# Performance work log

Hardware: AMD Instinct MI355X
Metric: run time of the kernel (lower is better)

Reference implementation:

```python
import jax, jax.numpy as jnp
import numpy as np

C = 1.0          # curvature (c_in == c_out)
MIN = 1e-15      # min_norm clamp (HGCN Hyperboloid)
PROJ_EPS = 4e-3  # proj eps for float32 (HGCN)
MAX_NORM = 1e3   # max tangent norm clamp in expmap
N, D = 262144, 256


def _proj(x, c):
    # project back onto hyperboloid: recompute time coordinate
    K = 1.0 / c
    y = x[..., 1:]
    x0 = jnp.sqrt(jnp.clip(K + jnp.sum(y * y, -1, keepdims=True), PROJ_EPS))
    return jnp.concatenate([x0, y], -1)


def _expmap0(u, c):
    sqrtK = (1.0 / c) ** 0.5
    d = u[..., 1:]
    n = jnp.clip(jnp.linalg.norm(d, axis=-1, keepdims=True), MIN)
    theta = n / sqrtK
    x = jnp.concatenate([sqrtK * jnp.cosh(theta), sqrtK * jnp.sinh(theta) * d / n], -1)
    return _proj(x, c)


def _logmap0(x, c):
    sqrtK = (1.0 / c) ** 0.5
    y = x[..., 1:]
    yn = jnp.clip(jnp.linalg.norm(y, axis=-1, keepdims=True), MIN)
    theta = jnp.arccosh(jnp.clip(x[..., :1] / sqrtK, 1.0 + 1e-7))
    return jnp.concatenate([jnp.zeros_like(theta), sqrtK * theta * y / yn], -1)


def _proj_tan(u, x, c):
    ux = jnp.sum(x[..., 1:] * u[..., 1:], -1, keepdims=True)
    u0 = ux / jnp.clip(x[..., :1], MIN)
    return jnp.concatenate([u0, u[..., 1:]], -1)


def _expmap(u, x, c):
    sqrtK = (1.0 / c) ** 0.5
    mdot = -u[..., :1] ** 2 + jnp.sum(u[..., 1:] ** 2, -1, keepdims=True)  # Minkowski <u,u>
    normu = jnp.minimum(jnp.sqrt(jnp.clip(mdot, 0.0)), MAX_NORM)
    theta = jnp.clip(normu / sqrtK, MIN)
    return _proj(jnp.cosh(theta) * x + jnp.sinh(theta) * u / theta, c)


def _transp0(x, u, c):
    # parallel transport of tangent u from the origin to x
    sqrtK = (1.0 / c) ** 0.5
    x0 = x[..., :1]
    y = x[..., 1:]
    yn = jnp.clip(jnp.linalg.norm(y, axis=-1, keepdims=True), MIN)
    yhat = y / yn
    v = jnp.concatenate([-yn, (sqrtK - x0) * yhat], -1)
    alpha = jnp.sum(yhat * u[..., 1:], -1, keepdims=True) / sqrtK
    return _proj_tan(u - alpha * v, x, c)


def _zero0(u):
    # proj_tan0: zero out the time coordinate
    return jnp.concatenate([jnp.zeros_like(u[..., :1]), u[..., 1:]], -1)


def _layernorm(t, g, b, eps=1e-5):
    mu = jnp.mean(t, -1, keepdims=True)
    var = jnp.var(t, -1, keepdims=True)
    return (t - mu) * jax.lax.rsqrt(var + eps) * g + b


def setup_inputs() -> dict:
    key = jax.random.key(0)
    k1, k2, k3, k4, k5 = jax.random.split(key, 5)
    # point on the hyperboloid: expmap0 of a tangent vector at origin
    u = 0.1 * jax.random.normal(k1, (N, D), dtype=jnp.float32)
    h = _expmap0(_zero0(u), C)
    # xavier_uniform with gain 0.25 for the linear weight
    bound = 0.25 * float(np.sqrt(6.0 / (D + D)))
    W = jax.random.uniform(k2, (D, D), dtype=jnp.float32, minval=-bound, maxval=bound)
    bias = 0.01 * jax.random.normal(k3, (1, D), dtype=jnp.float32)
    gamma = 1.0 + 0.1 * jax.random.normal(k4, (D - 1,), dtype=jnp.float32)
    beta = 0.01 * jax.random.normal(k5, (D - 1,), dtype=jnp.float32)
    return {"h": h, "W": W, "bias": bias, "gamma": gamma, "beta": beta}


def reference(h, W, bias, gamma, beta):
    # HypNorm: logmap0 -> LayerNorm over spatial dims -> expmap0
    t = _logmap0(h, C)
    t = jnp.concatenate([t[..., :1], _layernorm(t[..., 1:], gamma, beta)], -1)
    h1 = _expmap0(t, C)
    # HypLinear: logmap0 -> GEMM -> proj_tan0 -> expmap0 -> bias transport + expmap
    x = _logmap0(h1, C)
    x = x @ W.T
    x = _expmap0(_zero0(x), C)
    b = jnp.broadcast_to(bias, x.shape)
    b = _transp0(x, _zero0(b), C)
    res = _expmap(b, x, C)
    # HypAct: logmap0 -> relu -> proj_tan0 -> expmap0
    xt = jax.nn.relu(_logmap0(res, C))
    return _expmap0(_zero0(xt), C)
```

## Files before the change

kernel.cpp:

```cpp
#include <hip/hip_runtime.h>
#include <hip/hip_bf16.h>
#include <math.h>


#define MINV 1e-15f

typedef __bf16 bf16x8 __attribute__((ext_vector_type(8)));
typedef __bf16 bf16x4 __attribute__((ext_vector_type(4)));
typedef float floatx4 __attribute__((ext_vector_type(4)));

__global__ __launch_bounds__(256) void prep_kernel(const float* __restrict__ W,
                                                   const float* __restrict__ bias,
                                                   __bf16* __restrict__ Wb,
                                                   float* __restrict__ scal) {
  int b = blockIdx.x;
  if (b < 64) {
    int idx = b * 1024 + threadIdx.x * 4;
    int j = idx >> 8;
    float4 w;
    if (j < 255) w = *(const float4*)(W + idx + 256);
    else w = make_float4(0.f, 0.f, 0.f, 0.f);
    bf16x4 o;
    o[0] = (__bf16)w.x; o[1] = (__bf16)w.y; o[2] = (__bf16)w.z; o[3] = (__bf16)w.w;
    *(bf16x4*)(Wb + idx) = o;
  } else if (threadIdx.x < 64) {
    int l = threadIdx.x;
    float4 bv = *(const float4*)(bias + l * 4);
    float s = bv.x * bv.x + bv.y * bv.y + bv.z * bv.z + bv.w * bv.w;
    if (l == 0) s -= bv.x * bv.x;
    for (int m = 1; m < 64; m <<= 1) s += __shfl_xor(s, m);
    if (l == 0) {
      float nb = sqrtf(s);
      float normu = fminf(nb, 1000.0f);
      float th = fmaxf(normu, MINV);
      scal[0] = coshf(th);
      scal[1] = sinhf(th) / th;
      scal[2] = s;
    }
  }
}

__global__ __launch_bounds__(256, 4) void hnn_kernel(const float* __restrict__ h,
                                                     const __bf16* __restrict__ Wb,
                                                     const float* __restrict__ bias,
                                                     const float* __restrict__ gamma,
                                                     const float* __restrict__ beta,
                                                     const float* __restrict__ scal,
                                                     float* __restrict__ out) {
  __shared__ __bf16 Xs[64][264];
  __shared__ __align__(16) float gs[256];
  __shared__ __align__(16) float bs[256];
  __shared__ float partA[64][4];
  __shared__ float partB[64][4];
  __shared__ float rowAB[64][2];
  __shared__ float partX[64][4];
  __shared__ float rowS[64];

  const int tid = threadIdx.x;
  const int wave = tid >> 6;
  const int lane = tid & 63;
  const int lane16 = lane & 15;
  const int quad = lane >> 4;
  const int rowBlock = blockIdx.x * 64;

  float4 hv[4][4];
#pragma unroll
  for (int it = 0; it < 4; ++it) {
    const int row = rowBlock + wave * 16 + it * 4 + quad;
    const float4* hp = (const float4*)(h + row * 256 + lane16 * 16);
    hv[it][0] = hp[0]; hv[it][1] = hp[1]; hv[it][2] = hp[2]; hv[it][3] = hp[3];
  }

  if (tid < 255) { gs[tid + 1] = gamma[tid]; bs[tid + 1] = beta[tid]; }
  else { gs[0] = 0.f; bs[0] = 0.f; }
  __syncthreads();

  float4 gv[4], bv[4];
#pragma unroll
  for (int q = 0; q < 4; ++q) {
    gv[q] = *(const float4*)(gs + lane16 * 16 + q * 4);
    bv[q] = *(const float4*)(bs + lane16 * 16 + q * 4);
  }

#pragma unroll
  for (int it = 0; it < 4; ++it) {
    const int lrow = wave * 16 + it * 4 + quad;
    float vals[16] = {hv[it][0].x, hv[it][0].y, hv[it][0].z, hv[it][0].w,
                      hv[it][1].x, hv[it][1].y, hv[it][1].z, hv[it][1].w,
                      hv[it][2].x, hv[it][2].y, hv[it][2].z, hv[it][2].w,
                      hv[it][3].x, hv[it][3].y, hv[it][3].z, hv[it][3].w};
    float s1l = 0.f, s2l = 0.f;
#pragma unroll
    for (int i = 0; i < 16; ++i) { s1l += vals[i]; s2l += vals[i] * vals[i]; }
    if (lane16 == 0) { s1l -= vals[0]; s2l -= vals[0] * vals[0]; }
#pragma unroll
    for (int m = 1; m < 16; m <<= 1) {
      s1l += __shfl_xor(s1l, m);
      s2l += __shfl_xor(s2l, m);
    }
    float h0 = __shfl(vals[0], lane & 48);
    float yn = fmaxf(sqrtf(s2l), MINV);
    float xc = fmaxf(h0, 1.0f + 1e-7f);
    float theta = __logf(xc + sqrtf(xc * xc - 1.0f));
    float s = theta / yn;
    float mu = s * s1l * (1.0f / 255.0f);
    float var = s * s * (s2l * (1.0f / 255.0f)) - mu * mu;
    float rstd = rsqrtf(var + 1e-5f);
    float a = s * rstd;
    float bshift = -mu * rstd;
    bf16x8 o0, o1;
#pragma unroll
    for (int q = 0; q < 4; ++q) {
      float4 g4 = gv[q];
      float4 b4 = bv[q];
      float t0 = (a * vals[q * 4 + 0] + bshift) * g4.x + b4.x;
      float t1 = (a * vals[q * 4 + 1] + bshift) * g4.y + b4.y;
      float t2 = (a * vals[q * 4 + 2] + bshift) * g4.z + b4.z;
      float t3 = (a * vals[q * 4 + 3] + bshift) * g4.w + b4.w;
      if (q < 2) {
        o0[q * 4 + 0] = (__bf16)t0; o0[q * 4 + 1] = (__bf16)t1;
        o0[q * 4 + 2] = (__bf16)t2; o0[q * 4 + 3] = (__bf16)t3;
      } else {
        o1[(q - 2) * 4 + 0] = (__bf16)t0; o1[(q - 2) * 4 + 1] = (__bf16)t1;
        o1[(q - 2) * 4 + 2] = (__bf16)t2; o1[(q - 2) * 4 + 3] = (__bf16)t3;
      }
    }
    *(bf16x8*)(&Xs[lrow][lane16 * 16]) = o0;
    *(bf16x8*)(&Xs[lrow][lane16 * 16 + 8]) = o1;
  }
  __syncthreads();

  floatx4 acc[4][4];
#pragma unroll
  for (int rt = 0; rt < 4; ++rt)
#pragma unroll
    for (int jt = 0; jt < 4; ++jt) acc[rt][jt] = (floatx4){0.f, 0.f, 0.f, 0.f};

  const int colBase = wave * 64;
  const __bf16* wbase = Wb + (colBase + lane16) * 256 + quad * 8;
  const __bf16* xbase = &Xs[lane16][quad * 8];

#pragma unroll
  for (int kk = 0; kk < 8; ++kk) {
    bf16x8 bfr[4], afr[4];
#pragma unroll
    for (int jt = 0; jt < 4; ++jt)
      bfr[jt] = *(const bf16x8*)(wbase + jt * 4096 + kk * 32);
#pragma unroll
    for (int rt = 0; rt < 4; ++rt)
      afr[rt] = *(const bf16x8*)(xbase + rt * 4224 + kk * 32);
#pragma unroll
    for (int rt = 0; rt < 4; ++rt)
#pragma unroll
      for (int jt = 0; jt < 4; ++jt)
        acc[rt][jt] = __builtin_amdgcn_mfma_f32_16x16x32_bf16(afr[rt], bfr[jt],
                                                              acc[rt][jt], 0, 0, 0);
  }

  float bb1[4];
#pragma unroll
  for (int jt = 0; jt < 4; ++jt) {
    int c = colBase + jt * 16 + lane16;
    bb1[jt] = (c < 255) ? bias[c + 1] : 0.f;
  }

#pragma unroll
  for (int rt = 0; rt < 4; ++rt) {
#pragma unroll
    for (int e = 0; e < 4; ++e) {
      float sv2 = 0.f, svb = 0.f;
#pragma unroll
      for (int jt = 0; jt < 4; ++jt) {
        float v = acc[rt][jt][e];
        sv2 += v * v;
        svb += v * bb1[jt];
      }
#pragma unroll
      for (int m = 1; m < 16; m <<= 1) {
        sv2 += __shfl_xor(sv2, m);
        svb += __shfl_xor(svb, m);
      }
      if (lane16 == 0) {
        int r = rt * 16 + quad * 4 + e;
        partA[r][wave] = sv2;
        partB[r][wave] = svb;
      }
    }
  }
  __syncthreads();

  if (tid < 64) {
    float sv2 = partA[tid][0] + partA[tid][1] + partA[tid][2] + partA[tid][3];
    float svb = partB[tid][0] + partB[tid][1] + partB[tid][2] + partB[tid][3];
    const float c1 = scal[0];
    const float s1s = scal[1];
    const float tb2 = scal[2];
    float n = fmaxf(sqrtf(sv2), MINV);
    float inv_n = 1.0f / n;
    float alpha = svb * inv_n;
    float ex = __expf(n);
    float iex = 1.0f / ex;
    float ch = 0.5f * (ex + iex), sh = 0.5f * (ex - iex);
    float beta_ = c1 * sh + s1s * alpha * (ch - 1.0f);
    float rn2 = beta_ * beta_ + 2.0f * beta_ * s1s * alpha + s1s * s1s * tb2;
    float rn = sqrtf(fmaxf(rn2, 0.f));
    float res0 = sqrtf(1.0f + rn2);
    float th3 = __logf(res0 + rn);
    float sc3 = th3 / fmaxf(rn, MINV);
    rowAB[tid][0] = sc3 * beta_ * inv_n;
    rowAB[tid][1] = sc3 * s1s;
  }
  __syncthreads();

#pragma unroll
  for (int rt = 0; rt < 4; ++rt) {
#pragma unroll
    for (int e = 0; e < 4; ++e) {
      int r = rt * 16 + quad * 4 + e;
      float Ar = rowAB[r][0];
      float Br = rowAB[r][1];
      float sx2 = 0.f;
#pragma unroll
      for (int jt = 0; jt < 4; ++jt) {
        float x = fmaxf(Ar * acc[rt][jt][e] + Br * bb1[jt], 0.f);
        acc[rt][jt][e] = x;
        sx2 += x * x;
      }
#pragma unroll
      for (int m = 1; m < 16; m <<= 1) sx2 += __shfl_xor(sx2, m);
      if (lane16 == 0) partX[r][wave] = sx2;
    }
  }
  __syncthreads();

  if (tid < 64) {
    float sx2 = partX[tid][0] + partX[tid][1] + partX[tid][2] + partX[tid][3];
    float n2 = fmaxf(sqrtf(sx2), MINV);
    float e2 = __expf(n2);
    float ie2 = 1.0f / e2;
    rowS[tid] = 0.5f * (e2 - ie2) / n2;
    out[(size_t)(rowBlock + tid) * 256] = 0.5f * (e2 + ie2);
  }
  __syncthreads();

#pragma unroll
  for (int rt = 0; rt < 4; ++rt) {
#pragma unroll
    for (int e = 0; e < 4; ++e) {
      int r = rt * 16 + quad * 4 + e;
      float scl = rowS[r];
      float* orow = out + (size_t)(rowBlock + r) * 256;
#pragma unroll
      for (int jt = 0; jt < 4; ++jt) {
        int c = colBase + jt * 16 + lane16;
        if (c < 255) orow[c + 1] = scl * acc[rt][jt][e];
      }
    }
  }
}

extern "C" void kernel_launch(void* const* d_in, const int* in_sizes, int n_in,
                              void* d_out, int out_size, void* d_ws, size_t ws_size,
                              hipStream_t stream) {
  const float* h     = (const float*)d_in[0];
  const float* W     = (const float*)d_in[1];
  const float* bias  = (const float*)d_in[2];
  const float* gamma = (const float*)d_in[3];
  const float* beta  = (const float*)d_in[4];
  float* out = (float*)d_out;

  __bf16* Wb  = (__bf16*)d_ws;
  float* scal = (float*)((char*)d_ws + 131072);

  prep_kernel<<<dim3(65), dim3(256), 0, stream>>>(W, bias, Wb, scal);
  hnn_kernel<<<dim3(4096), dim3(256), 0, stream>>>(h, Wb, bias, gamma, beta, scal, out);
}
```

Before: 495.7 us.

## Process two row tiles per block, prefetching next tile's h during GEMM

Each block now handles two 64-row tiles, and part of the second tile's h rows are loaded during the first tile's MFMA and epilogue to overlap global loads with compute. Per-row scalars are now computed redundantly by every wave and broadcast with shuffles instead of being written by one wave to shared memory, which removes two barriers per tile. Gamma, beta, bias and the scalar reads are amortised over two tiles. In exchange, the grid is halved and register pressure rises from the held hv prefetch, which may reduce occupancy or latency hiding.

Measured after the change: 893.4 us. +80.2%, slower.

```diff
diff --git a/kernel.cpp b/kernel.cpp
--- a/kernel.cpp
+++ b/kernel.cpp
@@ -50,112 +50,20 @@
   __shared__ __bf16 Xs[64][264];
   __shared__ __align__(16) float gs[256];
   __shared__ __align__(16) float bs[256];
-  __shared__ float partA[64][4];
-  __shared__ float partB[64][4];
-  __shared__ float rowAB[64][2];
-  __shared__ float partX[64][4];
-  __shared__ float rowS[64];
+  __shared__ __align__(16) float partA[64][4];
+  __shared__ __align__(16) float partB[64][4];
+  __shared__ __align__(16) float partX[64][4];
 
   const int tid = threadIdx.x;
   const int wave = tid >> 6;
   const int lane = tid & 63;
   const int lane16 = lane & 15;
   const int quad = lane >> 4;
-  const int rowBlock = blockIdx.x * 64;
-
-  float4 hv[4][4];
-#pragma unroll
-  for (int it = 0; it < 4; ++it) {
-    const int row = rowBlock + wave * 16 + it * 4 + quad;
-    const float4* hp = (const float4*)(h + row * 256 + lane16 * 16);
-    hv[it][0] = hp[0]; hv[it][1] = hp[1]; hv[it][2] = hp[2]; hv[it][3] = hp[3];
-  }
+  const int tile0 = blockIdx.x * 2;
+  const int colBase = wave * 64;
 
   if (tid < 255) { gs[tid + 1] = gamma[tid]; bs[tid + 1] = beta[tid]; }
   else { gs[0] = 0.f; bs[0] = 0.f; }
-  __syncthreads();
-
-  float4 gv[4], bv[4];
-#pragma unroll
-  for (int q = 0; q < 4; ++q) {
-    gv[q] = *(const float4*)(gs + lane16 * 16 + q * 4);
-    bv[q] = *(const float4*)(bs + lane16 * 16 + q * 4);
-  }
-
-#pragma unroll
-  for (int it = 0; it < 4; ++it) {
-    const int lrow = wave * 16 + it * 4 + quad;
-    float vals[16] = {hv[it][0].x, hv[it][0].y, hv[it][0].z, hv[it][0].w,
-                      hv[it][1].x, hv[it][1].y, hv[it][1].z, hv[it][1].w,
-                      hv[it][2].x, hv[it][2].y, hv[it][2].z, hv[it][2].w,
-                      hv[it][3].x, hv[it][3].y, hv[it][3].z, hv[it][3].w};
-    float s1l = 0.f, s2l = 0.f;
-#pragma unroll
-    for (int i = 0; i < 16; ++i) { s1l += vals[i]; s2l += vals[i] * vals[i]; }
-    if (lane16 == 0) { s1l -= vals[0]; s2l -= vals[0] * vals[0]; }
-#pragma unroll
-    for (int m = 1; m < 16; m <<= 1) {
-      s1l += __shfl_xor(s1l, m);
-      s2l += __shfl_xor(s2l, m);
-    }
-    float h0 = __shfl(vals[0], lane & 48);
-    float yn = fmaxf(sqrtf(s2l), MINV);
-    float xc = fmaxf(h0, 1.0f + 1e-7f);
-    float theta = __logf(xc + sqrtf(xc * xc - 1.0f));
-    float s = theta / yn;
-    float mu = s * s1l * (1.0f / 255.0f);
-    float var = s * s * (s2l * (1.0f / 255.0f)) - mu * mu;
-    float rstd = rsqrtf(var + 1e-5f);
-    float a = s * rstd;
-    float bshift = -mu * rstd;
-    bf16x8 o0, o1;
-#pragma unroll
-    for (int q = 0; q < 4; ++q) {
-      float4 g4 = gv[q];
-      float4 b4 = bv[q];
-      float t0 = (a * vals[q * 4 + 0] + bshift) * g4.x + b4.x;
-      float t1 = (a * vals[q * 4 + 1] + bshift) * g4.y + b4.y;
-      float t2 = (a * vals[q * 4 + 2] + bshift) * g4.z + b4.z;
-      float t3 = (a * vals[q * 4 + 3] + bshift) * g4.w + b4.w;
-      if (q < 2) {
-        o0[q * 4 + 0] = (__bf16)t0; o0[q * 4 + 1] = (__bf16)t1;
-        o0[q * 4 + 2] = (__bf16)t2; o0[q * 4 + 3] = (__bf16)t3;
-      } else {
-        o1[(q - 2) * 4 + 0] = (__bf16)t0; o1[(q - 2) * 4 + 1] = (__bf16)t1;
-        o1[(q - 2) * 4 + 2] = (__bf16)t2; o1[(q - 2) * 4 + 3] = (__bf16)t3;
-      }
-    }
-    *(bf16x8*)(&Xs[lrow][lane16 * 16]) = o0;
-    *(bf16x8*)(&Xs[lrow][lane16 * 16 + 8]) = o1;
-  }
-  __syncthreads();
-
-  floatx4 acc[4][4];
-#pragma unroll
-  for (int rt = 0; rt < 4; ++rt)
-#pragma unroll
-    for (int jt = 0; jt < 4; ++jt) acc[rt][jt] = (floatx4){0.f, 0.f, 0.f, 0.f};
-
-  const int colBase = wave * 64;
-  const __bf16* wbase = Wb + (colBase + lane16) * 256 + quad * 8;
-  const __bf16* xbase = &Xs[lane16][quad * 8];
-
-#pragma unroll
-  for (int kk = 0; kk < 8; ++kk) {
-    bf16x8 bfr[4], afr[4];
-#pragma unroll
-    for (int jt = 0; jt < 4; ++jt)
-      bfr[jt] = *(const bf16x8*)(wbase + jt * 4096 + kk * 32);
-#pragma unroll
-    for (int rt = 0; rt < 4; ++rt)
-      afr[rt] = *(const bf16x8*)(xbase + rt * 4224 + kk * 32);
-#pragma unroll
-    for (int rt = 0; rt < 4; ++rt)
-#pragma unroll
-      for (int jt = 0; jt < 4; ++jt)
-        acc[rt][jt] = __builtin_amdgcn_mfma_f32_16x16x32_bf16(afr[rt], bfr[jt],
-                                                              acc[rt][jt], 0, 0, 0);
-  }
 
   float bb1[4];
 #pragma unroll
@@ -163,97 +71,212 @@
     int c = colBase + jt * 16 + lane16;
     bb1[jt] = (c < 255) ? bias[c + 1] : 0.f;
   }
-
-#pragma unroll
-  for (int rt = 0; rt < 4; ++rt) {
-#pragma unroll
-    for (int e = 0; e < 4; ++e) {
-      float sv2 = 0.f, svb = 0.f;
-#pragma unroll
-      for (int jt = 0; jt < 4; ++jt) {
-        float v = acc[rt][jt][e];
-        sv2 += v * v;
-        svb += v * bb1[jt];
-      }
-#pragma unroll
-      for (int m = 1; m < 16; m <<= 1) {
-        sv2 += __shfl_xor(sv2, m);
-        svb += __shfl_xor(svb, m);
-      }
-      if (lane16 == 0) {
-        int r = rt * 16 + quad * 4 + e;
-        partA[r][wave] = sv2;
-        partB[r][wave] = svb;
-      }
-    }
+  const float c1 = scal[0];
+  const float s1s = scal[1];
+  const float tb2 = scal[2];
+
+  float4 hv[4][4];
+#pragma unroll
+  for (int it = 0; it < 4; ++it) {
+    const size_t row = (size_t)(tile0 * 64 + wave * 16 + it * 4 + quad);
+    const float4* hp = (const float4*)(h + row * 256 + lane16 * 16);
+    hv[it][0] = hp[0]; hv[it][1] = hp[1]; hv[it][2] = hp[2]; hv[it][3] = hp[3];
   }
   __syncthreads();
 
-  if (tid < 64) {
-    float sv2 = partA[tid][0] + partA[tid][1] + partA[tid][2] + partA[tid][3];
-    float svb = partB[tid][0] + partB[tid][1] + partB[tid][2] + partB[tid][3];
-    const float c1 = scal[0];
-    const float s1s = scal[1];
-    const float tb2 = scal[2];
-    float n = fmaxf(sqrtf(sv2), MINV);
-    float inv_n = 1.0f / n;
-    float alpha = svb * inv_n;
-    float ex = __expf(n);
-    float iex = 1.0f / ex;
-    float ch = 0.5f * (ex + iex), sh = 0.5f * (ex - iex);
-    float beta_ = c1 * sh + s1s * alpha * (ch - 1.0f);
-    float rn2 = beta_ * beta_ + 2.0f * beta_ * s1s * alpha + s1s * s1s * tb2;
-    float rn = sqrtf(fmaxf(rn2, 0.f));
-    float res0 = sqrtf(1.0f + rn2);
-    float th3 = __logf(res0 + rn);
-    float sc3 = th3 / fmaxf(rn, MINV);
-    rowAB[tid][0] = sc3 * beta_ * inv_n;
-    rowAB[tid][1] = sc3 * s1s;
-  }
-  __syncthreads();
-
-#pragma unroll
-  for (int rt = 0; rt < 4; ++rt) {
-#pragma unroll
-    for (int e = 0; e < 4; ++e) {
-      int r = rt * 16 + quad * 4 + e;
-      float Ar = rowAB[r][0];
-      float Br = rowAB[r][1];
-      float sx2 = 0.f;
-#pragma unroll
-      for (int jt = 0; jt < 4; ++jt) {
-        float x = fmaxf(Ar * acc[rt][jt][e] + Br * bb1[jt], 0.f);
-        acc[rt][jt][e] = x;
-        sx2 += x * x;
-      }
-#pragma unroll
-      for (int m = 1; m < 16; m <<= 1) sx2 += __shfl_xor(sx2, m);
-      if (lane16 == 0) partX[r][wave] = sx2;
-    }
-  }
-  __syncthreads();
-
-  if (tid < 64) {
-    float sx2 = partX[tid][0] + partX[tid][1] + partX[tid][2] + partX[tid][3];
-    float n2 = fmaxf(sqrtf(sx2), MINV);
-    float e2 = __expf(n2);
-    float ie2 = 1.0f / e2;
-    rowS[tid] = 0.5f * (e2 - ie2) / n2;
-    out[(size_t)(rowBlock + tid) * 256] = 0.5f * (e2 + ie2);
-  }
-  __syncthreads();
-
-#pragma unroll
-  for (int rt = 0; rt < 4; ++rt) {
-#pragma unroll
-    for (int e = 0; e < 4; ++e) {
-      int r = rt * 16 + quad * 4 + e;
-      float scl = rowS[r];
-      float* orow = out + (size_t)(rowBlock + r) * 256;
-#pragma unroll
-      for (int jt = 0; jt < 4; ++jt) {
-        int c = colBase + jt * 16 + lane16;
-        if (c < 255) orow[c + 1] = scl * acc[rt][jt][e];
+  const __bf16* wbase = Wb + (colBase + lane16) * 256 + quad * 8;
+  const __bf16* xbase = &Xs[lane16][quad * 8];
+
+  for (int t = 0; t < 2; ++t) {
+    const int rowBlock = (tile0 + t) * 64;
+
+    if (t == 1) {
+#pragma unroll
+      for (int it = 2; it < 4; ++it) {
+        const size_t row = (size_t)(rowBlock + wave * 16 + it * 4 + quad);
+        const float4* hp = (const float4*)(h + row * 256 + lane16 * 16);
+        hv[it][0] = hp[0]; hv[it][1] = hp[1]; hv[it][2] = hp[2]; hv[it][3] = hp[3];
+      }
+    }
+
+    float4 gv[4], bvv[4];
+#pragma unroll
+    for (int q = 0; q < 4; ++q) {
+      gv[q] = *(const float4*)(gs + lane16 * 16 + q * 4);
+      bvv[q] = *(const float4*)(bs + lane16 * 16 + q * 4);
+    }
+
+#pragma unroll
+    for (int it = 0; it < 4; ++it) {
+      const int lrow = wave * 16 + it * 4 + quad;
+      float vals[16] = {hv[it][0].x, hv[it][0].y, hv[it][0].z, hv[it][0].w,
+                        hv[it][1].x, hv[it][1].y, hv[it][1].z, hv[it][1].w,
+                        hv[it][2].x, hv[it][2].y, hv[it][2].z, hv[it][2].w,
+                        hv[it][3].x, hv[it][3].y, hv[it][3].z, hv[it][3].w};
+      float s1l = 0.f, s2l = 0.f;
+#pragma unroll
+      for (int i = 0; i < 16; ++i) { s1l += vals[i]; s2l += vals[i] * vals[i]; }
+      if (lane16 == 0) { s1l -= vals[0]; s2l -= vals[0] * vals[0]; }
+#pragma unroll
+      for (int m = 1; m < 16; m <<= 1) {
+        s1l += __shfl_xor(s1l, m);
+        s2l += __shfl_xor(s2l, m);
+      }
+      float h0 = __shfl(vals[0], lane & 48);
+      float yn = fmaxf(sqrtf(s2l), MINV);
+      float xc = fmaxf(h0, 1.0f + 1e-7f);
+      float theta = __logf(xc + sqrtf(xc * xc - 1.0f));
+      float s = theta / yn;
+      float mu = s * s1l * (1.0f / 255.0f);
+      float var = s * s * (s2l * (1.0f / 255.0f)) - mu * mu;
+      float rstd = rsqrtf(var + 1e-5f);
+      float a = s * rstd;
+      float bshift = -mu * rstd;
+      bf16x8 o0, o1;
+#pragma unroll
+      for (int q = 0; q < 4; ++q) {
+        float4 g4 = gv[q];
+        float4 b4 = bvv[q];
+        float t0 = (a * vals[q * 4 + 0] + bshift) * g4.x + b4.x;
+        float t1 = (a * vals[q * 4 + 1] + bshift) * g4.y + b4.y;
+        float t2 = (a * vals[q * 4 + 2] + bshift) * g4.z + b4.z;
+        float t3 = (a * vals[q * 4 + 3] + bshift) * g4.w + b4.w;
+        if (q < 2) {
+          o0[q * 4 + 0] = (__bf16)t0; o0[q * 4 + 1] = (__bf16)t1;
+          o0[q * 4 + 2] = (__bf16)t2; o0[q * 4 + 3] = (__bf16)t3;
+        } else {
+          o1[(q - 2) * 4 + 0] = (__bf16)t0; o1[(q - 2) * 4 + 1] = (__bf16)t1;
+          o1[(q - 2) * 4 + 2] = (__bf16)t2; o1[(q - 2) * 4 + 3] = (__bf16)t3;
+        }
+      }
+      *(bf16x8*)(&Xs[lrow][lane16 * 16]) = o0;
+      *(bf16x8*)(&Xs[lrow][lane16 * 16 + 8]) = o1;
+    }
+    __syncthreads();
+
+    floatx4 acc[4][4];
+#pragma unroll
+    for (int rt = 0; rt < 4; ++rt)
+#pragma unroll
+      for (int jt = 0; jt < 4; ++jt) acc[rt][jt] = (floatx4){0.f, 0.f, 0.f, 0.f};
+
+#pragma unroll
+    for (int kk = 0; kk < 8; ++kk) {
+      bf16x8 bfr[4], afr[4];
+#pragma unroll
+      for (int jt = 0; jt < 4; ++jt)
+        bfr[jt] = *(const bf16x8*)(wbase + jt * 4096 + kk * 32);
+#pragma unroll
+      for (int rt = 0; rt < 4; ++rt)
+        afr[rt] = *(const bf16x8*)(xbase + rt * 4224 + kk * 32);
+#pragma unroll
+      for (int rt = 0; rt < 4; ++rt)
+#pragma unroll
+        for (int jt = 0; jt < 4; ++jt)
+          acc[rt][jt] = __builtin_amdgcn_mfma_f32_16x16x32_bf16(afr[rt], bfr[jt],
+                                                                acc[rt][jt], 0, 0, 0);
+    }
+
+    if (t == 0) {
+#pragma unroll
+      for (int it = 0; it < 2; ++it) {
+        const size_t row = (size_t)(rowBlock + 64 + wave * 16 + it * 4 + quad);
+        const float4* hp = (const float4*)(h + row * 256 + lane16 * 16);
+        hv[it][0] = hp[0]; hv[it][1] = hp[1]; hv[it][2] = hp[2]; hv[it][3] = hp[3];
+      }
+    }
+
+#pragma unroll
+    for (int rt = 0; rt < 4; ++rt) {
+#pragma unroll
+      for (int e = 0; e < 4; ++e) {
+        float sv2 = 0.f, svb = 0.f;
+#pragma unroll
+        for (int jt = 0; jt < 4; ++jt) {
+          float v = acc[rt][jt][e];
+          sv2 += v * v;
+          svb += v * bb1[jt];
+        }
+#pragma unroll
+        for (int m = 1; m < 16; m <<= 1) {
+          sv2 += __shfl_xor(sv2, m);
+          svb += __shfl_xor(svb, m);
+        }
+        if (lane16 == 0) {
+          int r = rt * 16 + quad * 4 + e;
+          partA[r][wave] = sv2;
+          partB[r][wave] = svb;
+        }
+      }
+    }
+    __syncthreads();
+
+    float Ar_me, Br_me;
+    {
+      float4 pa = *(const float4*)&partA[lane][0];
+      float4 pb = *(const float4*)&partB[lane][0];
+      float sv2 = pa.x + pa.y + pa.z + pa.w;
+      float svb = pb.x + pb.y + pb.z + pb.w;
+      float n = fmaxf(sqrtf(sv2), MINV);
+      float inv_n = 1.0f / n;
+      float alpha = svb * inv_n;
+      float ex = __expf(n);
+      float iex = 1.0f / ex;
+      float ch = 0.5f * (ex + iex), sh = 0.5f * (ex - iex);
+      float beta_ = c1 * sh + s1s * alpha * (ch - 1.0f);
+      float rn2 = beta_ * beta_ + 2.0f * beta_ * s1s * alpha + s1s * s1s * tb2;
+      float rn = sqrtf(fmaxf(rn2, 0.f));
+      float res0 = sqrtf(1.0f + rn2);
+      float th3 = __logf(res0 + rn);
+      float sc3 = th3 / fmaxf(rn, MINV);
+      Ar_me = sc3 * beta_ * inv_n;
+      Br_me = sc3 * s1s;
+    }
+
+#pragma unroll
+    for (int rt = 0; rt < 4; ++rt) {
+#pragma unroll
+      for (int e = 0; e < 4; ++e) {
+        int src = rt * 16 + quad * 4 + e;
+        float Ar = __shfl(Ar_me, src);
+        float Br = __shfl(Br_me, src);
+        float sx2 = 0.f;
+#pragma unroll
+        for (int jt = 0; jt < 4; ++jt) {
+          float x = fmaxf(Ar * acc[rt][jt][e] + Br * bb1[jt], 0.f);
+          acc[rt][jt][e] = x;
+          sx2 += x * x;
+        }
+#pragma unroll
+        for (int m = 1; m < 16; m <<= 1) sx2 += __shfl_xor(sx2, m);
+        if (lane16 == 0) partX[src][wave] = sx2;
+      }
+    }
+    __syncthreads();
+
+    float rowS_me;
+    {
+      float4 px = *(const float4*)&partX[lane][0];
+      float sx2 = px.x + px.y + px.z + px.w;
+      float n2 = fmaxf(sqrtf(sx2), MINV);
+      float e2 = __expf(n2);
+      float ie2 = 1.0f / e2;
+      rowS_me = 0.5f * (e2 - ie2) / n2;
+      if (wave == 0) out[(size_t)(rowBlock + lane) * 256] = 0.5f * (e2 + ie2);
+    }
+
+#pragma unroll
+    for (int rt = 0; rt < 4; ++rt) {
+#pragma unroll
+      for (int e = 0; e < 4; ++e) {
+        int src = rt * 16 + quad * 4 + e;
+        float scl = __shfl(rowS_me, src);
+        float* orow = out + (size_t)(rowBlock + src) * 256;
+#pragma unroll
+        for (int jt = 0; jt < 4; ++jt) {
+          int c = colBase + jt * 16 + lane16;
+          if (c < 255) orow[c + 1] = scl * acc[rt][jt][e];
+        }
       }
     }
   }
@@ -273,5 +296,5 @@
   float* scal = (float*)((char*)d_ws + 131072);
 
   prep_kernel<<<dim3(65), dim3(256), 0, stream>>>(W, bias, Wb, scal);
-  hnn_kernel<<<dim3(4096), dim3(256), 0, stream>>>(h, Wb, bias, gamma, beta, scal, out);
+  hnn_kernel<<<dim3(2048), dim3(256), 0, stream>>>(h, Wb, bias, gamma, beta, scal, out);
 }
```
